# Optimization experiments

Measured on AMD Instinct MI355X. Metric: run time of the kernel, lower is better.

The kernel has to match this reference:

```python
import jax, jax.numpy as jnp
import numpy as np

V, E, H, O = 32000, 512, 1024, 8   # vocab, embed_dim, hidden_dim, output_dim
B, T = 64, 512
PAD = 1  # padding_idx=1 in nn.Embedding


def setup_inputs() -> dict:
    key = jax.random.key(0)
    ks = jax.random.split(key, 8)
    s = 1.0 / np.sqrt(H)  # torch LSTM init scale
    x = jax.random.randint(ks[0], (B, T), 0, V)
    W_emb = jax.random.normal(ks[1], (V, E), dtype=jnp.float32)
    W_emb = W_emb.at[PAD].set(0.0)  # padding row is zero
    W_ih = jax.random.uniform(ks[2], (4 * H, E), jnp.float32, -s, s)
    W_hh = jax.random.uniform(ks[3], (4 * H, H), jnp.float32, -s, s)
    b_ih = jax.random.uniform(ks[4], (4 * H,), jnp.float32, -s, s)
    b_hh = jax.random.uniform(ks[5], (4 * H,), jnp.float32, -s, s)
    W_out = jax.random.uniform(ks[6], (O, H), jnp.float32, -s, s)
    b_out = jax.random.uniform(ks[7], (O,), jnp.float32, -s, s)
    return {"x": x, "W_emb": W_emb, "W_ih": W_ih, "W_hh": W_hh,
            "b_ih": b_ih, "b_hh": b_hh, "W_out": W_out, "b_out": b_out}


def _lstm_scan(emb_tbe, W_ih, W_hh, b_ih, b_hh):
    # emb_tbe: [T, B, E] -> hidden states [T, B, H]; torch gate order i,f,g,o
    Hh = W_hh.shape[1]
    b = b_ih + b_hh

    def step(carry, x_t):
        h, c = carry
        z = x_t @ W_ih.T + h @ W_hh.T + b  # [B, 4H]
        i, f, g, o = jnp.split(z, 4, axis=-1)
        c = jax.nn.sigmoid(f) * c + jax.nn.sigmoid(i) * jnp.tanh(g)
        h = jax.nn.sigmoid(o) * jnp.tanh(c)
        return (h, c), h

    h0 = jnp.zeros((emb_tbe.shape[1], Hh), emb_tbe.dtype)
    _, hs = jax.lax.scan(step, (h0, h0), emb_tbe)
    return hs


def reference(x, W_emb, W_ih, W_hh, b_ih, b_hh, W_out, b_out):
    Bsz = x.shape[0]
    emb = W_emb[x]                                   # [B, T, E]
    hs = _lstm_scan(emb.transpose(1, 0, 2), W_ih, W_hh, b_ih, b_hh)
    outputs = hs.transpose(1, 0, 2)                  # [B, T, H]
    pad = (x == PAD)
    outputs = jnp.where(pad[..., None], 0.0, outputs)  # masked_fill_
    lengths = jnp.sum(~pad, axis=1)                  # non-pad token counts
    final = outputs[jnp.arange(Bsz), lengths - 1]    # [B, H]
    # Dropout(p=0.5) is identity in eval mode
    logits = final @ W_out.T + b_out                 # [B, O]
    return logits
```

## Files before the change

kernel.cpp:

```cpp
#include <hip/hip_runtime.h>

typedef short bf16x8 __attribute__((ext_vector_type(8)));
typedef float f32x4  __attribute__((ext_vector_type(4)));
typedef unsigned long long u64;

#define MFMA16(a, b, c) __builtin_amdgcn_mfma_f32_16x16x32_bf16((a), (b), (c), 0, 0, 0)
#define AT_LD(p, o)    __hip_atomic_load((p), (o), __HIP_MEMORY_SCOPE_AGENT)
#define AT_ST(p, v, o) __hip_atomic_store((p), (v), (o), __HIP_MEMORY_SCOPE_AGENT)
#define AT_ADD(p, v, o) __hip_atomic_fetch_add((p), (v), (o), __HIP_MEMORY_SCOPE_AGENT)

#define HSLOT 67584

__device__ __forceinline__ unsigned short f2bf(float f) {
  union { float f; unsigned u; } v; v.f = f;
  unsigned u = v.u;
  u += 0x7fffu + ((u >> 16) & 1u);
  return (unsigned short)(u >> 16);
}
__device__ __forceinline__ float bf2f(unsigned short h) {
  union { unsigned u; float f; } v; v.u = ((unsigned)h) << 16;
  return v.f;
}
__device__ __forceinline__ float sigf(float x) { return 1.f / (1.f + __expf(-x)); }
__device__ __forceinline__ float tanh_(float x) {
  x = fminf(15.f, fmaxf(-15.f, x));
  float e = __expf(2.f * x);
  return (e - 1.f) / (e + 1.f);
}

__device__ __forceinline__ void flagbar(unsigned* bar, int wg, unsigned target) {
  unsigned* gen = bar + 8192;
  __syncthreads();
  if (threadIdx.x == 0) {
    asm volatile("" ::: "memory");
    AT_ST(bar + wg * 64, target, __ATOMIC_RELAXED);
  }
  if (wg == 0) {
    if (threadIdx.x < 128) {
      while (AT_LD(bar + threadIdx.x * 64, __ATOMIC_RELAXED) < target)
        __builtin_amdgcn_s_sleep(1);
    }
    __syncthreads();
    if (threadIdx.x == 0) AT_ST(gen, target, __ATOMIC_RELAXED);
  } else {
    if (threadIdx.x == 0) {
      while (AT_LD(gen, __ATOMIC_RELAXED) < target) __builtin_amdgcn_s_sleep(1);
    }
  }
  __syncthreads();
}

__device__ __forceinline__ void gbar_gemm(unsigned* bar, unsigned target) {
  __syncthreads();
  if (threadIdx.x == 0) {
    unsigned arr = AT_ADD(bar + 8256, 1u, __ATOMIC_RELEASE);
    if (arr == target * 128u - 1u) AT_ST(bar + 8320, target, __ATOMIC_RELEASE);
    while (AT_LD(bar + 8320, __ATOMIC_RELAXED) < target) __builtin_amdgcn_s_sleep(4);
    asm volatile("" ::: "memory");
  }
  __syncthreads();
}

__global__ void k_conv(const float* __restrict__ wih, const float* __restrict__ whh,
                       const float* __restrict__ wemb,
                       unsigned short* __restrict__ oih, unsigned short* __restrict__ ohh,
                       unsigned short* __restrict__ oemb) {
  const size_t NIH = (size_t)4096 * 512, NHH = (size_t)4096 * 1024;
  const size_t NE = (size_t)32000 * 512;
  size_t i0 = ((size_t)blockIdx.x * blockDim.x + threadIdx.x) * 4;
  size_t gs = (size_t)gridDim.x * blockDim.x * 4;
  for (size_t j = i0; j < NIH; j += gs) {
    float4 v = *(const float4*)(wih + j);
    uint2 pk;
    pk.x = (unsigned)f2bf(v.x) | ((unsigned)f2bf(v.y) << 16);
    pk.y = (unsigned)f2bf(v.z) | ((unsigned)f2bf(v.w) << 16);
    *(uint2*)(oih + j) = pk;
  }
  for (size_t j = i0; j < NHH; j += gs) {
    float4 v = *(const float4*)(whh + j);
    uint2 pk;
    pk.x = (unsigned)f2bf(v.x) | ((unsigned)f2bf(v.y) << 16);
    pk.y = (unsigned)f2bf(v.z) | ((unsigned)f2bf(v.w) << 16);
    *(uint2*)(ohh + j) = pk;
  }
  if (oemb)
    for (size_t j = i0; j < NE; j += gs) {
      float4 v = *(const float4*)(wemb + j);
      uint2 pk;
      pk.x = (unsigned)f2bf(v.x) | ((unsigned)f2bf(v.y) << 16);
      pk.y = (unsigned)f2bf(v.z) | ((unsigned)f2bf(v.w) << 16);
      *(uint2*)(oemb + j) = pk;
    }
}

__global__ void k_tsel(const int* __restrict__ x, int* __restrict__ tsel,
                       int* __restrict__ padsel) {
  int b = threadIdx.x >> 3, j = threadIdx.x & 7;
  int c = 0;
  for (int t = j * 64; t < j * 64 + 64; ++t) c += (x[b * 512 + t] != 1) ? 1 : 0;
  c += __shfl_xor(c, 1);
  c += __shfl_xor(c, 2);
  c += __shfl_xor(c, 4);
  if (j == 0) {
    int ts = (c - 1) & 511;
    tsel[b] = ts;
    padsel[b] = (x[b * 512 + ts] == 1) ? 1 : 0;
  }
}

__global__ void k_logits(const float* __restrict__ finalb, const float* __restrict__ Wout,
                         const float* __restrict__ bout, float* __restrict__ out) {
  int tid = threadIdx.x;
  for (int e = tid; e < 512; e += 256) {
    int b = e >> 3, o = e & 7;
    const float* f = finalb + (size_t)b * 1024;
    const float* w = Wout + (size_t)o * 1024;
    float s = 0.f;
    for (int k = 0; k < 1024; ++k) s += f[k] * w[k];
    out[e] = s + bout[o];
  }
}

struct SmemT {
  unsigned short sW[32][1032];
  union {
    struct { unsigned short A[128][72]; unsigned short Bt[256][72]; } g;
    struct { float z[64][33]; } rec;
    struct { unsigned short zs[128][136]; } zst;
  } u;
};

__global__ __launch_bounds__(256, 1) void k_main(
    const int* __restrict__ x, const float* __restrict__ Wemb,
    const float* __restrict__ bih, const float* __restrict__ bhh,
    const unsigned short* __restrict__ Wihb, const unsigned short* __restrict__ Whhb,
    const unsigned short* __restrict__ wembb,
    unsigned short* __restrict__ hr, float* __restrict__ finalb,
    const int* __restrict__ tsel, const int* __restrict__ padsel,
    unsigned short* __restrict__ zxr, unsigned* __restrict__ bar, int chunkT,
    int nslot) {
  __shared__ SmemT smem;
  const int wg = blockIdx.x, tid = threadIdx.x;
  const int wave = tid >> 6, lane = tid & 63;
  const int l15 = lane & 15, lg = lane >> 4;
  unsigned* gemm_done = bar + 8384;
  unsigned* rec_done  = bar + 8448;
  const f32x4 fz = {0.f, 0.f, 0.f, 0.f};
  const int nChunks = 512 / chunkT;
  const size_t slotE = (size_t)chunkT * 64 * 4096;

  if (wg < 128) {
    for (int e = tid; e < 32 * 128; e += 256) {
      int n = e >> 7, kq = (e & 127) << 3;
      int grow = (n >> 3) * 1024 + wg * 8 + (n & 7);
      *(uint4*)&smem.sW[n][kq] = *(const uint4*)(Whhb + (size_t)grow * 1024 + kq);
    }
    const int q = tid & 3;
    const int my_b = tid >> 2;
    const int zc = wg * 8 + 2 * q;
    float biasv[4][2];
#pragma unroll
    for (int g = 0; g < 4; ++g)
#pragma unroll
      for (int c = 0; c < 2; ++c)
        biasv[g][c] = bih[g * 1024 + zc + c] + bhh[g * 1024 + zc + c];
    const int my_tsel = tsel[my_b];
    const int my_pad = padsel[my_b];
    const size_t hwe = (size_t)((my_b >> 4) * 32 + (wg >> 2)) * 512 +
                       (size_t)(wg & 3) * 128 + (size_t)(my_b & 15) * 8 + 2 * q;
    float cc0 = 0.f, cc1 = 0.f;
    unsigned bt = 0;
    AT_ST((unsigned*)hr + (wg * 256 + tid), 0u, __ATOMIC_RELAXED);
    flagbar(bar, wg, ++bt);

    for (int ch = 0; ch < nChunks; ++ch) {
      const int t0 = ch * chunkT;
      const unsigned short* zxbase = zxr + (size_t)(ch % nslot) * slotE;
      if (tid == 0) {
        while (AT_LD(gemm_done, __ATOMIC_RELAXED) < (unsigned)(ch + 1))
          __builtin_amdgcn_s_sleep(2);
        (void)AT_LD(gemm_done, __ATOMIC_ACQUIRE);
        asm volatile("" ::: "memory");
      }
      __syncthreads();
      union { uint2 u2[2]; unsigned short s[8]; } vv;
      {
        const unsigned short* zr = zxbase + (size_t)my_b * 4096 + zc * 4;
        vv.u2[0] = *(const uint2*)zr;
        vv.u2[1] = *(const uint2*)(zr + 4);
      }
      for (int tl = 0; tl < chunkT; ++tl) {
        const int t = t0 + tl;
        const unsigned short* hp =
            hr + (size_t)(t & 15) * HSLOT + (size_t)wave * 16384 + (size_t)lane * 8;
        f32x4 r0 = fz, r1 = fz;
        bf16x8 af[32];
#pragma unroll
        for (int j = 0; j < 32; ++j) af[j] = *(const bf16x8*)(hp + (size_t)j * 512);
#pragma unroll
        for (int j = 0; j < 32; ++j) {
          int ks = j * 32;
          bf16x8 b0 = *(const bf16x8*)&smem.sW[l15][ks + (lg << 3)];
          bf16x8 b1 = *(const bf16x8*)&smem.sW[16 + l15][ks + (lg << 3)];
          r0 = MFMA16(af[j], b0, r0);
          r1 = MFMA16(af[j], b1, r1);
        }
#pragma unroll
        for (int r = 0; r < 4; ++r) {
          smem.u.rec.z[wave * 16 + (lg << 2) + r][l15] = r0[r];
          smem.u.rec.z[wave * 16 + (lg << 2) + r][16 + l15] = r1[r];
        }
        __syncthreads();
        int hc = 2 * q;
        float zi0 = smem.u.rec.z[my_b][hc]          + biasv[0][0] + bf2f(vv.s[0]);
        float zf0 = smem.u.rec.z[my_b][8 + hc]      + biasv[1][0] + bf2f(vv.s[1]);
        float zg0 = smem.u.rec.z[my_b][16 + hc]     + biasv[2][0] + bf2f(vv.s[2]);
        float zo0 = smem.u.rec.z[my_b][24 + hc]     + biasv[3][0] + bf2f(vv.s[3]);
        float zi1 = smem.u.rec.z[my_b][hc + 1]      + biasv[0][1] + bf2f(vv.s[4]);
        float zf1 = smem.u.rec.z[my_b][8 + hc + 1]  + biasv[1][1] + bf2f(vv.s[5]);
        float zg1 = smem.u.rec.z[my_b][16 + hc + 1] + biasv[2][1] + bf2f(vv.s[6]);
        float zo1 = smem.u.rec.z[my_b][24 + hc + 1] + biasv[3][1] + bf2f(vv.s[7]);
        cc0 = sigf(zf0) * cc0 + sigf(zi0) * tanh_(zg0);
        cc1 = sigf(zf1) * cc1 + sigf(zi1) * tanh_(zg1);
        float h0 = sigf(zo0) * tanh_(cc0);
        float h1 = sigf(zo1) * tanh_(cc1);
        if (t == my_tsel) {
          finalb[(size_t)my_b * 1024 + zc]     = my_pad ? 0.f : h0;
          finalb[(size_t)my_b * 1024 + zc + 1] = my_pad ? 0.f : h1;
        }
        unsigned hp32 = (unsigned)f2bf(h0) | ((unsigned)f2bf(h1) << 16);
        AT_ST((unsigned*)(hr + (size_t)((t + 1) & 15) * HSLOT + hwe), hp32,
              __ATOMIC_RELAXED);
        if (tl + 1 < chunkT) {
          const unsigned short* zn =
              zxbase + (size_t)((tl + 1) * 64 + my_b) * 4096 + zc * 4;
          vv.u2[0] = *(const uint2*)zn;
          vv.u2[1] = *(const uint2*)(zn + 4);
        }
        flagbar(bar, wg, ++bt);
      }
      if (wg == 0 && tid == 0) AT_ST(rec_done, (unsigned)(ch + 1), __ATOMIC_RELAXED);
    }
  } else {
    const int gw = wg - 128;
    unsigned gt = 0;
    for (int ch = 0; ch < nChunks; ++ch) {
      if (tid == 0 && ch >= nslot) {
        while (AT_LD(rec_done, __ATOMIC_RELAXED) < (unsigned)(ch - nslot + 1))
          __builtin_amdgcn_s_sleep(8);
        asm volatile("" ::: "memory");
      }
      __syncthreads();
      const int t0 = ch * chunkT;
      unsigned short* zx = zxr + (size_t)(ch % nslot) * slotE;
      const int pmN = chunkT >> 1;
      const int npatch = pmN * 16;
      for (int p = gw; p < npatch; p += 128) {
        const int pm = p % pmN;
        const int n0 = (p / pmN) * 256;
        f32x4 acc[8][4];
#pragma unroll
        for (int mt = 0; mt < 8; ++mt)
#pragma unroll
          for (int nt = 0; nt < 4; ++nt) acc[mt][nt] = fz;
        for (int kc = 0; kc < 512; kc += 64) {
          __syncthreads();
          {
            int r = tid >> 1, half = (tid & 1) << 5;
            int tl = pm * 2 + (r >> 6), b = r & 63;
            int erow = x[b * 512 + t0 + tl];
            if (wembb) {
              const unsigned short* srcp = wembb + (size_t)erow * 512 + kc + half;
#pragma unroll
              for (int j = 0; j < 32; j += 8)
                *(uint4*)&smem.u.g.A[r][half + j] = *(const uint4*)(srcp + j);
            } else {
              const float* srcp = Wemb + (size_t)erow * 512 + kc + half;
#pragma unroll
              for (int j = 0; j < 32; j += 4) {
                float4 v = *(const float4*)(srcp + j);
                uint2 pk;
                pk.x = (unsigned)f2bf(v.x) | ((unsigned)f2bf(v.y) << 16);
                pk.y = (unsigned)f2bf(v.z) | ((unsigned)f2bf(v.w) << 16);
                *(uint2*)&smem.u.g.A[r][half + j] = pk;
              }
            }
          }
          {
            int zcx = n0 + tid;
            int wrow = (zcx & 3) * 1024 + (zcx >> 2);
            const unsigned short* srcp = Wihb + (size_t)wrow * 512 + kc;
#pragma unroll
            for (int j = 0; j < 64; j += 8)
              *(uint4*)&smem.u.g.Bt[tid][j] = *(const uint4*)(srcp + j);
          }
          __syncthreads();
#pragma unroll
          for (int ks = 0; ks < 64; ks += 32) {
            bf16x8 af[8];
#pragma unroll
            for (int mt = 0; mt < 8; ++mt)
              af[mt] = *(const bf16x8*)&smem.u.g.A[mt * 16 + l15][ks + (lg << 3)];
#pragma unroll
            for (int nt = 0; nt < 4; ++nt) {
              bf16x8 bfr =
                  *(const bf16x8*)&smem.u.g.Bt[(wave * 4 + nt) * 16 + l15][ks + (lg << 3)];
#pragma unroll
              for (int mt = 0; mt < 8; ++mt)
                acc[mt][nt] = MFMA16(af[mt], bfr, acc[mt][nt]);
            }
          }
        }
#pragma unroll
        for (int h = 0; h < 2; ++h) {
          __syncthreads();
          if ((wave >> 1) == h) {
#pragma unroll
            for (int mt = 0; mt < 8; ++mt)
#pragma unroll
              for (int nt = 0; nt < 4; ++nt)
#pragma unroll
                for (int r = 0; r < 4; ++r)
                  smem.u.zst.zs[mt * 16 + (lg << 2) + r][(wave & 1) * 64 + nt * 16 + l15] =
                      f2bf(acc[mt][nt][r]);
          }
          __syncthreads();
          int m = tid >> 1, qq = (tid & 1) << 6;
          int tl2 = pm * 2 + (m >> 6), bb = m & 63;
          unsigned short* dst = zx + ((size_t)(tl2 * 64 + bb)) * 4096 + n0 + h * 128 + qq;
#pragma unroll
          for (int j = 0; j < 64; j += 8)
            *(uint4*)(dst + j) = *(const uint4*)&smem.u.zst.zs[m][qq + j];
        }
      }
      gbar_gemm(bar, ++gt);
      if (wg == 128 && tid == 0) AT_ST(gemm_done, gt, __ATOMIC_RELAXED);
    }
  }
}

extern "C" void kernel_launch(void* const* d_in, const int* in_sizes, int n_in,
                              void* d_out, int out_size, void* d_ws, size_t ws_size,
                              hipStream_t stream) {
  (void)in_sizes; (void)n_in; (void)out_size;
  const int*   x    = (const int*)  d_in[0];
  const float* Wemb = (const float*)d_in[1];
  const float* Wih  = (const float*)d_in[2];
  const float* Whh  = (const float*)d_in[3];
  const float* bih  = (const float*)d_in[4];
  const float* bhh  = (const float*)d_in[5];
  const float* Wout = (const float*)d_in[6];
  const float* bout = (const float*)d_in[7];
  float* out = (float*)d_out;
  char* ws = (char*)d_ws;

  constexpr size_t OFF_WIH = 0;
  constexpr size_t OFF_WHH = OFF_WIH + (size_t)4096 * 512 * 2;
  constexpr size_t OFF_HR  = OFF_WHH + (size_t)4096 * 1024 * 2;
  constexpr size_t OFF_FIN = OFF_HR + (size_t)16 * HSLOT * 2;
  constexpr size_t OFF_TS  = OFF_FIN + (size_t)64 * 1024 * 4;
  constexpr size_t OFF_PS  = OFF_TS + 4096;
  constexpr size_t OFF_BAR = OFF_PS + 4096;
  constexpr size_t OFF_WEB = OFF_BAR + 40960;
  constexpr size_t WEB_SZ  = (size_t)32000 * 512 * 2;
  constexpr size_t SLOT_SZ = (size_t)16 * 64 * 4096 * 2;

  int chunkT = 16;
  bool wbf = true;
  int nslot = 2;
  if (OFF_WEB + WEB_SZ + 2 * SLOT_SZ <= ws_size) {
    nslot = (int)((ws_size - OFF_WEB - WEB_SZ) / SLOT_SZ);
    if (nslot > 32) nslot = 32;
  } else if (OFF_WEB + 2 * SLOT_SZ <= ws_size) {
    wbf = false;
    nslot = (int)((ws_size - OFF_WEB) / SLOT_SZ);
    if (nslot > 32) nslot = 32;
  } else {
    wbf = false;
    while (chunkT > 2 &&
           OFF_WEB + (size_t)2 * chunkT * 64 * 4096 * 2 > ws_size)
      chunkT >>= 1;
  }
  const size_t OFF_ZX = OFF_WEB + (wbf ? WEB_SZ : 0);

  unsigned short* wihb  = (unsigned short*)(ws + OFF_WIH);
  unsigned short* whhb  = (unsigned short*)(ws + OFF_WHH);
  unsigned short* hr    = (unsigned short*)(ws + OFF_HR);
  float* finalb         = (float*)(ws + OFF_FIN);
  int* tsel             = (int*)(ws + OFF_TS);
  int* padsel           = (int*)(ws + OFF_PS);
  unsigned* bar         = (unsigned*)(ws + OFF_BAR);
  unsigned short* wembb = wbf ? (unsigned short*)(ws + OFF_WEB) : (unsigned short*)nullptr;
  unsigned short* zxr   = (unsigned short*)(ws + OFF_ZX);

  hipMemsetAsync(ws + OFF_BAR, 0, 40960, stream);
  k_conv<<<2048, 256, 0, stream>>>(Wih, Whh, Wemb, wihb, whhb, wembb);
  k_tsel<<<1, 512, 0, stream>>>(x, tsel, padsel);
  k_main<<<256, 256, 0, stream>>>(x, Wemb, bih, bhh, wihb, whhb, wembb, hr, finalb,
                                  tsel, padsel, zxr, bar, chunkT, nslot);
  k_logits<<<1, 256, 0, stream>>>(finalb, Wout, bout, out);
}
```

Baseline: 3.235 ms.

## Replace centralized grid barrier with decentralized per-block flag polling in recurrence

The recurrence blocks no longer go through a two-level grid barrier, where block 0 gathers every arrival flag and publishes a generation counter. Instead, wave 0 of every block polls all 128 per-block flags directly with a wave-wide vote, then releases the block's other waves through a shared-memory token. This removes one global round trip and the serialization through block 0 at each timestep. In exchange, polling traffic on the flag cache lines rises 128-fold, and the relaxed atomics with no fences may weaken memory ordering for the h data.

```diff
diff --git a/kernel.cpp b/kernel.cpp
--- a/kernel.cpp
+++ b/kernel.cpp
@@ -8,6 +8,8 @@
 #define AT_LD(p, o)    __hip_atomic_load((p), (o), __HIP_MEMORY_SCOPE_AGENT)
 #define AT_ST(p, v, o) __hip_atomic_store((p), (v), (o), __HIP_MEMORY_SCOPE_AGENT)
 #define AT_ADD(p, v, o) __hip_atomic_fetch_add((p), (v), (o), __HIP_MEMORY_SCOPE_AGENT)
+#define WG_LD(p) __hip_atomic_load((p), __ATOMIC_RELAXED, __HIP_MEMORY_SCOPE_WORKGROUP)
+#define WG_ST(p, v) __hip_atomic_store((p), (v), __ATOMIC_RELAXED, __HIP_MEMORY_SCOPE_WORKGROUP)
 
 #define HSLOT 67584
 
@@ -26,28 +28,6 @@
   x = fminf(15.f, fmaxf(-15.f, x));
   float e = __expf(2.f * x);
   return (e - 1.f) / (e + 1.f);
-}
-
-__device__ __forceinline__ void flagbar(unsigned* bar, int wg, unsigned target) {
-  unsigned* gen = bar + 8192;
-  __syncthreads();
-  if (threadIdx.x == 0) {
-    asm volatile("" ::: "memory");
-    AT_ST(bar + wg * 64, target, __ATOMIC_RELAXED);
-  }
-  if (wg == 0) {
-    if (threadIdx.x < 128) {
-      while (AT_LD(bar + threadIdx.x * 64, __ATOMIC_RELAXED) < target)
-        __builtin_amdgcn_s_sleep(1);
-    }
-    __syncthreads();
-    if (threadIdx.x == 0) AT_ST(gen, target, __ATOMIC_RELAXED);
-  } else {
-    if (threadIdx.x == 0) {
-      while (AT_LD(gen, __ATOMIC_RELAXED) < target) __builtin_amdgcn_s_sleep(1);
-    }
-  }
-  __syncthreads();
 }
 
 __device__ __forceinline__ void gbar_gemm(unsigned* bar, unsigned target) {
@@ -122,6 +102,7 @@
 }
 
 struct SmemT {
+  unsigned tok;
   unsigned short sW[32][1032];
   union {
     struct { unsigned short A[128][72]; unsigned short Bt[256][72]; } g;
@@ -150,6 +131,7 @@
   const size_t slotE = (size_t)chunkT * 64 * 4096;
 
   if (wg < 128) {
+    if (tid == 0) smem.tok = 0;
     for (int e = tid; e < 32 * 128; e += 256) {
       int n = e >> 7, kq = (e & 127) << 3;
       int grow = (n >> 3) * 1024 + wg * 8 + (n & 7);
@@ -169,9 +151,10 @@
     const size_t hwe = (size_t)((my_b >> 4) * 32 + (wg >> 2)) * 512 +
                        (size_t)(wg & 3) * 128 + (size_t)(my_b & 15) * 8 + 2 * q;
     float cc0 = 0.f, cc1 = 0.f;
-    unsigned bt = 0;
+
     AT_ST((unsigned*)hr + (wg * 256 + tid), 0u, __ATOMIC_RELAXED);
-    flagbar(bar, wg, ++bt);
+    __syncthreads();
+    if (tid == 0) AT_ST(bar + wg * 64, 1u, __ATOMIC_RELAXED);
 
     for (int ch = 0; ch < nChunks; ++ch) {
       const int t0 = ch * chunkT;
@@ -191,6 +174,23 @@
       }
       for (int tl = 0; tl < chunkT; ++tl) {
         const int t = t0 + tl;
+        const unsigned need = (unsigned)t + 1u;
+
+        if (wave == 0) {
+          const unsigned* f0 = bar + (lane * 2) * 64;
+          const unsigned* f1 = bar + (lane * 2 + 1) * 64;
+          for (;;) {
+            int ok = (AT_LD(f0, __ATOMIC_RELAXED) >= need) &&
+                     (AT_LD(f1, __ATOMIC_RELAXED) >= need);
+            if (__all(ok)) break;
+            __builtin_amdgcn_s_sleep(1);
+          }
+          if (lane == 0) WG_ST(&smem.tok, need);
+        } else {
+          while (WG_LD(&smem.tok) < need) __builtin_amdgcn_s_sleep(1);
+        }
+        asm volatile("" ::: "memory");
+
         const unsigned short* hp =
             hr + (size_t)(t & 15) * HSLOT + (size_t)wave * 16384 + (size_t)lane * 8;
         f32x4 r0 = fz, r1 = fz;
@@ -237,7 +237,8 @@
           vv.u2[0] = *(const uint2*)zn;
           vv.u2[1] = *(const uint2*)(zn + 4);
         }
-        flagbar(bar, wg, ++bt);
+        __syncthreads();
+        if (tid == 0) AT_ST(bar + wg * 64, need + 1u, __ATOMIC_RELAXED);
       }
       if (wg == 0 && tid == 0) AT_ST(rec_done, (unsigned)(ch + 1), __ATOMIC_RELAXED);
     }
```

New measurement: 3.269 ms. About the same (+1.0%).
